# Optimization experiments

Hardware: AMD Instinct MI355X
Metric: run time of the kernel (lower is better)

The kernel has to match this reference:

```python
import jax, jax.numpy as jnp
import numpy as np

N_NODES = 50000
N_EDGES = 800000
D = 128


def setup_inputs() -> dict:
    key = jax.random.key(0)
    ks = jax.random.split(key, 8)
    x = jax.random.normal(ks[0], (N_NODES, D), dtype=jnp.float32)
    src = jax.random.randint(ks[1], (N_EDGES,), 0, N_NODES, dtype=jnp.int64)
    dst = jax.random.randint(ks[2], (N_EDGES,), 0, N_NODES, dtype=jnp.int64)
    edge_weights = jax.random.uniform(ks[3], (N_EDGES,), dtype=jnp.float32)
    scale = 1.0 / np.sqrt(D)
    W1 = jax.random.normal(ks[4], (D, D), dtype=jnp.float32) * scale
    b1 = jnp.zeros((D,), dtype=jnp.float32)
    W2 = jax.random.normal(ks[5], (D, D), dtype=jnp.float32) * scale
    b2 = jnp.zeros((D,), dtype=jnp.float32)
    return {"x": x, "src": src, "dst": dst, "edge_weights": edge_weights,
            "W1": W1, "b1": b1, "W2": W2, "b2": b2}


def reference(x, src, dst, edge_weights, W1, b1, W2, b2):
    n_nodes = x.shape[0]
    # out-degrees (edges where node is the source), clamped to >= 1
    deg = jax.ops.segment_sum(jnp.ones_like(src, dtype=x.dtype), src,
                              num_segments=n_nodes)
    deg = jnp.maximum(deg, 1.0)
    # per-edge symmetric-normalization coefficient: 1/sqrt(deg_u * deg_v)
    coef = jax.lax.rsqrt(deg[src] * deg[dst]) * edge_weights  # [E]
    # gather-multiply-scatter: sum_{u->v} x[u] * coef into node v
    msgs = x[src] * coef[:, None]                              # [E, D]
    agg = jax.ops.segment_sum(msgs, dst, num_segments=n_nodes)  # [N, D]
    # FFN: Linear -> ReLU -> Linear (dropout = 0)
    h = jax.nn.relu(agg @ W1 + b1)
    return h @ W2 + b2
```

## Files before the change

kernel.cpp:

```cpp
#include <hip/hip_runtime.h>

#define NN 50000
#define NE 800000
#define D  128
#define HB 128
#define CH 6272
#define PW 50176
#define XB 128
#define RB 49

typedef short short8 __attribute__((ext_vector_type(8)));
typedef float f32x4  __attribute__((ext_vector_type(4)));
typedef unsigned char u8;

__device__ __forceinline__ ushort f2bf(float f) {
    union { float f; unsigned u; } v; v.f = f;
    unsigned r = v.u + 0x7FFFu + ((v.u >> 16) & 1u);
    return (ushort)(r >> 16);
}


__global__ __launch_bounds__(1024) void prep_kernel(const int* __restrict__ src,
                                                    const int* __restrict__ dst,
                                                    const float* __restrict__ x,
                                                    const float* __restrict__ W1,
                                                    const float* __restrict__ W2,
                                                    u8* __restrict__ psrc,
                                                    u8* __restrict__ pdst,
                                                    ushort* __restrict__ xbf,
                                                    ushort* __restrict__ W1t,
                                                    ushort* __restrict__ W2t) {
    __shared__ unsigned bins[2 * PW / 4];
    const int t = threadIdx.x, b = blockIdx.x;

    if (b < HB) {
        for (int i = t; i < 2 * PW / 16; i += 1024)
            ((uint4*)bins)[i] = make_uint4(0, 0, 0, 0);
        __syncthreads();
        const int base = b * CH;
#pragma unroll
        for (int i = 0; i < 2; ++i) {
            int e0 = base + i * 4096 + t * 4;
            if (e0 < base + CH && e0 < NE) {
                int4 s4 = *(const int4*)(src + e0);
                int4 d4 = *(const int4*)(dst + e0);
                atomicAdd(&bins[s4.x >> 2], 1u << ((s4.x & 3) << 3));
                atomicAdd(&bins[s4.y >> 2], 1u << ((s4.y & 3) << 3));
                atomicAdd(&bins[s4.z >> 2], 1u << ((s4.z & 3) << 3));
                atomicAdd(&bins[s4.w >> 2], 1u << ((s4.w & 3) << 3));
                atomicAdd(&bins[PW / 4 + (d4.x >> 2)], 1u << ((d4.x & 3) << 3));
                atomicAdd(&bins[PW / 4 + (d4.y >> 2)], 1u << ((d4.y & 3) << 3));
                atomicAdd(&bins[PW / 4 + (d4.z >> 2)], 1u << ((d4.z & 3) << 3));
                atomicAdd(&bins[PW / 4 + (d4.w >> 2)], 1u << ((d4.w & 3) << 3));
            }
        }
        __syncthreads();
        uint4* os = (uint4*)(psrc + (size_t)b * PW);
        uint4* od = (uint4*)(pdst + (size_t)b * PW);
        for (int i = t; i < PW / 16; i += 1024) {
            os[i] = ((const uint4*)bins)[i];
            od[i] = ((const uint4*)(bins + PW / 4))[i];
        }
    } else if (b < HB + 4) {
        int c = (b - HB) * 1024 + t;
        if (c < 4096) {
            const float* W = (c < 2048) ? W1 : W2;
            ushort* Wt     = (c < 2048) ? W1t : W2t;
            int cc = c & 2047;
            int n  = cc >> 4;
            int k0 = (cc & 15) * 8;
            ushort tmp[8];
#pragma unroll
            for (int j = 0; j < 8; ++j) tmp[j] = f2bf(W[(k0 + j) * D + n]);
            *reinterpret_cast<uint4*>(Wt + n * D + k0) = *reinterpret_cast<uint4*>(tmp);
        }
    } else {
        for (int i = (b - HB - 4) * 1024 + t; i < NN * D / 8; i += XB * 1024) {
            const float4* p = (const float4*)(x + (size_t)i * 8);
            float4 v0 = p[0], v1 = p[1];
            ushort tmp[8];
            tmp[0] = f2bf(v0.x); tmp[1] = f2bf(v0.y); tmp[2] = f2bf(v0.z); tmp[3] = f2bf(v0.w);
            tmp[4] = f2bf(v1.x); tmp[5] = f2bf(v1.y); tmp[6] = f2bf(v1.z); tmp[7] = f2bf(v1.w);
            *reinterpret_cast<uint4*>(xbf + (size_t)i * 8) = *reinterpret_cast<uint4*>(tmp);
        }
    }
}

__global__ __launch_bounds__(256) void xprep_kernel(const float* __restrict__ x,
                                                    ushort* __restrict__ xbf) {
    int i = blockIdx.x * 256 + threadIdx.x;
    if (i >= NN * D / 8) return;
    const float4* p = (const float4*)(x + (size_t)i * 8);
    float4 v0 = p[0], v1 = p[1];
    ushort tmp[8];
    tmp[0] = f2bf(v0.x); tmp[1] = f2bf(v0.y); tmp[2] = f2bf(v0.z); tmp[3] = f2bf(v0.w);
    tmp[4] = f2bf(v1.x); tmp[5] = f2bf(v1.y); tmp[6] = f2bf(v1.z); tmp[7] = f2bf(v1.w);
    *reinterpret_cast<uint4*>(xbf + (size_t)i * 8) = *reinterpret_cast<uint4*>(tmp);
}


__global__ __launch_bounds__(256) void reduce_kernel(const unsigned* __restrict__ psrc32,
                                                     unsigned* __restrict__ pdst32,
                                                     float* __restrict__ rsq,
                                                     int* __restrict__ cnt,
                                                     int* __restrict__ bsum49) {
    __shared__ int sm[256];
    int t = threadIdx.x;
    int g = blockIdx.x * 256 + t;
    unsigned s02 = 0, s13 = 0;
    for (int b = 0; b < HB; ++b) {
        unsigned w = psrc32[(size_t)b * (PW / 4) + g];
        s02 += w & 0x00FF00FFu;
        s13 += (w >> 8) & 0x00FF00FFu;
    }
    unsigned r02 = 0, r13 = 0;
    for (int b = 0; b < HB; ++b) {
        size_t idx = (size_t)b * (PW / 4) + g;
        unsigned w = pdst32[idx];
        pdst32[idx] = (r02 & 0xFFu) | ((r13 & 0xFFu) << 8) |
                      (r02 & 0x00FF0000u) | ((r13 & 0x00FF0000u) << 8);
        r02 += w & 0x00FF00FFu;
        r13 += (w >> 8) & 0x00FF00FFu;
    }
    int v0 = g * 4;
    int dg[4] = { (int)(s02 & 0xFFFFu), (int)(s13 & 0xFFFFu),
                  (int)(s02 >> 16),     (int)(s13 >> 16) };
    int ct[4] = { (int)(r02 & 0xFFFFu), (int)(r13 & 0xFFFFu),
                  (int)(r02 >> 16),     (int)(r13 >> 16) };
    if (v0 + 3 < NN) {
        float4 rq = make_float4(rsqrtf(fmaxf((float)dg[0], 1.f)),
                                rsqrtf(fmaxf((float)dg[1], 1.f)),
                                rsqrtf(fmaxf((float)dg[2], 1.f)),
                                rsqrtf(fmaxf((float)dg[3], 1.f)));
        *(float4*)(rsq + v0) = rq;
        *(int4*)(cnt + v0) = make_int4(ct[0], ct[1], ct[2], ct[3]);
    } else {
        for (int j = 0; j < 4; ++j)
            if (v0 + j < NN) {
                rsq[v0 + j] = rsqrtf(fmaxf((float)dg[j], 1.f));
                cnt[v0 + j] = ct[j];
            }
    }
    int pad_ok = (v0 + 3 < NN);
    int mysum = pad_ok ? (ct[0] + ct[1] + ct[2] + ct[3]) : 0;
    if (!pad_ok)
        for (int j = 0; j < 4; ++j) if (v0 + j < NN) mysum += ct[j];
    sm[t] = mysum;
    __syncthreads();
    for (int s = 128; s > 0; s >>= 1) {
        if (t < s) sm[t] += sm[t + s];
        __syncthreads();
    }
    if (t == 0) bsum49[blockIdx.x] = sm[0];
}

__global__ __launch_bounds__(256) void scan_bsum(int* __restrict__ bsum49) {
    __shared__ int sm[256];
    int t = threadIdx.x;
    int v = (t < RB) ? bsum49[t] : 0;
    sm[t] = v;
    __syncthreads();
    for (int d2 = 1; d2 < 256; d2 <<= 1) {
        int u = (t >= d2) ? sm[t - d2] : 0;
        __syncthreads();
        sm[t] += u;
        __syncthreads();
    }
    if (t < RB) bsum49[t] = sm[t] - v;
}

__global__ __launch_bounds__(1024) void scan_write(const int* __restrict__ cnt,
                                                   const int* __restrict__ bsum49,
                                                   int* __restrict__ offs) {
    __shared__ int sm[1024];
    int b = blockIdx.x, t = threadIdx.x;
    int i = b * 1024 + t;
    int v = (i < NN) ? cnt[i] : 0;
    sm[t] = v;
    __syncthreads();
    for (int d2 = 1; d2 < 1024; d2 <<= 1) {
        int u = (t >= d2) ? sm[t - d2] : 0;
        __syncthreads();
        sm[t] += u;
        __syncthreads();
    }
    if (i < NN) offs[i] = bsum49[b] + sm[t] - v;
    if (b == 0 && t == 0) offs[NN] = NE;
}


__global__ __launch_bounds__(1024) void scatter_kernel(const int* __restrict__ src,
                                                       const int* __restrict__ dst,
                                                       const float* __restrict__ ew,
                                                       const float* __restrict__ rsq,
                                                       const int* __restrict__ offs,
                                                       const u8* __restrict__ pd,
                                                       unsigned* __restrict__ csr) {
    __shared__ unsigned cur[PW / 4];
    const int t = threadIdx.x, b = blockIdx.x;
    for (int i = t; i < PW / 16; i += 1024)
        ((uint4*)cur)[i] = make_uint4(0, 0, 0, 0);
    __syncthreads();

    const u8* pdrow = pd + (size_t)b * PW;
    const int base = b * CH;
#pragma unroll
    for (int i = 0; i < 2; ++i) {
        int e0 = base + i * 4096 + t * 4;
        if (e0 < base + CH && e0 < NE) {
            int4 s4 = *(const int4*)(src + e0);
            int4 d4 = *(const int4*)(dst + e0);
            float4 w4 = *(const float4*)(ew + e0);
#pragma unroll
            for (int j = 0; j < 4; ++j) {
                int s = (j == 0) ? s4.x : (j == 1) ? s4.y : (j == 2) ? s4.z : s4.w;
                int d = (j == 0) ? d4.x : (j == 1) ? d4.y : (j == 2) ? d4.z : d4.w;
                float w = (j == 0) ? w4.x : (j == 1) ? w4.y : (j == 2) ? w4.z : w4.w;
                int sh = (d & 3) << 3;
                unsigned old = atomicAdd(&cur[d >> 2], 1u << sh);
                int rel = (int)((old >> sh) & 0xFFu);
                int pos = offs[d] + (int)pdrow[d] + rel;
                float coef = rsq[s] * rsq[d] * w;
                csr[pos] = (unsigned)s | ((unsigned)f2bf(coef) << 16);
            }
        }
    }
}


__device__ __forceinline__ void acc_row(unsigned e, int lane,
                                        const ushort* __restrict__ xbf,
                                        float& a0, float& a1, float& a2, float& a3) {
    float c = __int_as_float(e & 0xFFFF0000u);
    uint2 u = ((const uint2*)(xbf + (size_t)(e & 0xFFFFu) * D))[lane];
    a0 = fmaf(__int_as_float((int)(u.x << 16)),        c, a0);
    a1 = fmaf(__int_as_float((int)(u.x & 0xFFFF0000u)), c, a1);
    a2 = fmaf(__int_as_float((int)(u.y << 16)),        c, a2);
    a3 = fmaf(__int_as_float((int)(u.y & 0xFFFF0000u)), c, a3);
}

__global__ __launch_bounds__(256) void gather_bf16_kernel(const int* __restrict__ offs,
                                                          const unsigned* __restrict__ csr,
                                                          const ushort* __restrict__ xbf,
                                                          float* __restrict__ agg) {
    int v = blockIdx.x * 8 + (threadIdx.x >> 5);
    if (v >= NN) return;
    int lane = threadIdx.x & 31;
    int beg = offs[v], end = offs[v + 1];
    float a0 = 0.f, a1 = 0.f, a2 = 0.f, a3 = 0.f;
    for (int i0 = beg; i0 < end; i0 += 32) {
        int n = end - i0; if (n > 32) n = 32;
        unsigned ej = (lane < n) ? csr[i0 + lane] : 0u;
        int j = 0;
        for (; j + 3 < n; j += 4) {
            unsigned e0 = __shfl(ej, j,     32);
            unsigned e1 = __shfl(ej, j + 1, 32);
            unsigned e2 = __shfl(ej, j + 2, 32);
            unsigned e3 = __shfl(ej, j + 3, 32);
            const uint2* r0 = (const uint2*)(xbf + (size_t)(e0 & 0xFFFFu) * D);
            const uint2* r1 = (const uint2*)(xbf + (size_t)(e1 & 0xFFFFu) * D);
            const uint2* r2 = (const uint2*)(xbf + (size_t)(e2 & 0xFFFFu) * D);
            const uint2* r3 = (const uint2*)(xbf + (size_t)(e3 & 0xFFFFu) * D);
            uint2 u0 = r0[lane], u1 = r1[lane], u2 = r2[lane], u3 = r3[lane];
            float c0 = __int_as_float(e0 & 0xFFFF0000u);
            float c1 = __int_as_float(e1 & 0xFFFF0000u);
            float c2 = __int_as_float(e2 & 0xFFFF0000u);
            float c3 = __int_as_float(e3 & 0xFFFF0000u);
            a0 = fmaf(__int_as_float((int)(u0.x << 16)),         c0, a0);
            a1 = fmaf(__int_as_float((int)(u0.x & 0xFFFF0000u)), c0, a1);
            a2 = fmaf(__int_as_float((int)(u0.y << 16)),         c0, a2);
            a3 = fmaf(__int_as_float((int)(u0.y & 0xFFFF0000u)), c0, a3);
            a0 = fmaf(__int_as_float((int)(u1.x << 16)),         c1, a0);
            a1 = fmaf(__int_as_float((int)(u1.x & 0xFFFF0000u)), c1, a1);
            a2 = fmaf(__int_as_float((int)(u1.y << 16)),         c1, a2);
            a3 = fmaf(__int_as_float((int)(u1.y & 0xFFFF0000u)), c1, a3);
            a0 = fmaf(__int_as_float((int)(u2.x << 16)),         c2, a0);
            a1 = fmaf(__int_as_float((int)(u2.x & 0xFFFF0000u)), c2, a1);
            a2 = fmaf(__int_as_float((int)(u2.y << 16)),         c2, a2);
            a3 = fmaf(__int_as_float((int)(u2.y & 0xFFFF0000u)), c2, a3);
            a0 = fmaf(__int_as_float((int)(u3.x << 16)),         c3, a0);
            a1 = fmaf(__int_as_float((int)(u3.x & 0xFFFF0000u)), c3, a1);
            a2 = fmaf(__int_as_float((int)(u3.y << 16)),         c3, a2);
            a3 = fmaf(__int_as_float((int)(u3.y & 0xFFFF0000u)), c3, a3);
        }
        for (; j < n; ++j) {
            unsigned e = __shfl(ej, j, 32);
            acc_row(e, lane, xbf, a0, a1, a2, a3);
        }
    }
    ((float4*)(agg + (size_t)v * D))[lane] = make_float4(a0, a1, a2, a3);
}


__global__ __launch_bounds__(256) void ffn_mfma_kernel(const float* __restrict__ agg,
                                                       const ushort* __restrict__ W1t,
                                                       const ushort* __restrict__ W2t,
                                                       const float* __restrict__ b1,
                                                       const float* __restrict__ b2,
                                                       float* __restrict__ out) {
    __shared__ ushort Wt[128 * 128];
    __shared__ ushort hS[4][16 * 128];

    const int t  = threadIdx.x;
    const int w  = t >> 6;
    const int l  = t & 63;
    const int lr = l & 15;
    const int lk = l >> 4;
    const int r0 = blockIdx.x * 64;

    for (int i = 0; i < 8; ++i) {
        int c = i * 256 + t;
        int n = c >> 4;
        int slot = c & 15;
        uint4 v = ((const uint4*)W1t)[c];
        int byte = n * 256 + ((slot * 16) ^ ((n & 7) << 4));
        *(uint4*)((char*)Wt + byte) = v;
    }

    const int arow = r0 + w * 16 + lr;
    short8 afrag[4];
#pragma unroll
    for (int kb = 0; kb < 4; ++kb) {
        int k = kb * 32 + lk * 8;
        float4 v0 = make_float4(0.f, 0.f, 0.f, 0.f), v1 = v0;
        if (arow < NN) {
            const float4* ap = (const float4*)(agg + (size_t)arow * D + k);
            v0 = ap[0]; v1 = ap[1];
        }
        short8 a;
        a[0] = (short)f2bf(v0.x); a[1] = (short)f2bf(v0.y);
        a[2] = (short)f2bf(v0.z); a[3] = (short)f2bf(v0.w);
        a[4] = (short)f2bf(v1.x); a[5] = (short)f2bf(v1.y);
        a[6] = (short)f2bf(v1.z); a[7] = (short)f2bf(v1.w);
        afrag[kb] = a;
    }
    __syncthreads();

    f32x4 acc[8];
#pragma unroll
    for (int nt = 0; nt < 8; ++nt) acc[nt] = (f32x4){0.f, 0.f, 0.f, 0.f};
#pragma unroll
    for (int kb = 0; kb < 4; ++kb) {
        int kbyte = (kb * 32 + lk * 8) * 2;
#pragma unroll
        for (int nt = 0; nt < 8; ++nt) {
            int n = nt * 16 + lr;
            short8 b = *(const short8*)((const char*)Wt + n * 256 + (kbyte ^ ((n & 7) << 4)));
            acc[nt] = __builtin_amdgcn_mfma_f32_16x16x32_bf16(afrag[kb], b, acc[nt], 0, 0, 0);
        }
    }
#pragma unroll
    for (int nt = 0; nt < 8; ++nt) {
        int col = nt * 16 + lr;
        float bb = b1[col];
#pragma unroll
        for (int r = 0; r < 4; ++r) {
            int row = lk * 4 + r;
            float h = fmaxf(acc[nt][r] + bb, 0.0f);
            int byte = row * 256 + ((col * 2) ^ ((row & 7) << 4));
            *(ushort*)((char*)&hS[w][0] + byte) = f2bf(h);
        }
    }
    __syncthreads();

    for (int i = 0; i < 8; ++i) {
        int c = i * 256 + t;
        int n = c >> 4;
        int slot = c & 15;
        uint4 v = ((const uint4*)W2t)[c];
        int byte = n * 256 + ((slot * 16) ^ ((n & 7) << 4));
        *(uint4*)((char*)Wt + byte) = v;
    }
    __syncthreads();

    short8 hfrag[4];
#pragma unroll
    for (int kb = 0; kb < 4; ++kb) {
        int kbyte = (kb * 32 + lk * 8) * 2;
        hfrag[kb] = *(const short8*)((const char*)&hS[w][0] + lr * 256 + (kbyte ^ ((lr & 7) << 4)));
    }
#pragma unroll
    for (int nt = 0; nt < 8; ++nt) acc[nt] = (f32x4){0.f, 0.f, 0.f, 0.f};
#pragma unroll
    for (int kb = 0; kb < 4; ++kb) {
        int kbyte = (kb * 32 + lk * 8) * 2;
#pragma unroll
        for (int nt = 0; nt < 8; ++nt) {
            int n = nt * 16 + lr;
            short8 b = *(const short8*)((const char*)Wt + n * 256 + (kbyte ^ ((n & 7) << 4)));
            acc[nt] = __builtin_amdgcn_mfma_f32_16x16x32_bf16(hfrag[kb], b, acc[nt], 0, 0, 0);
        }
    }
#pragma unroll
    for (int nt = 0; nt < 8; ++nt) {
        int col = nt * 16 + lr;
        float bb = b2[col];
#pragma unroll
        for (int r = 0; r < 4; ++r) {
            int row = r0 + w * 16 + lk * 4 + r;
            if (row < NN) out[(size_t)row * D + col] = acc[nt][r] + bb;
        }
    }
}


extern "C" void kernel_launch(void* const* d_in, const int* in_sizes, int n_in,
                              void* d_out, int out_size, void* d_ws, size_t ws_size,
                              hipStream_t stream) {
    const float* x  = (const float*)d_in[0];
    const int* src  = (const int*)d_in[1];
    const int* dst  = (const int*)d_in[2];
    const float* ew = (const float*)d_in[3];
    const float* W1 = (const float*)d_in[4];
    const float* b1 = (const float*)d_in[5];
    const float* W2 = (const float*)d_in[6];
    const float* b2 = (const float*)d_in[7];
    float* out = (float*)d_out;

    char* base = (char*)d_ws;
    size_t off = 0;
    auto alloc = [&](size_t bytes) { char* p = base + off; off = (off + bytes + 15) & ~(size_t)15; return p; };
    u8* psrc      = (u8*)alloc((size_t)HB * PW);
    u8* pdst      = (u8*)alloc((size_t)HB * PW);
    float* rsq    = (float*)alloc((size_t)NN * 4);
    int* cnt      = (int*)alloc((size_t)NN * 4);
    int* offs     = (int*)alloc((size_t)(NN + 1) * 4);
    int* bsum49   = (int*)alloc((size_t)RB * 4);
    unsigned* csr = (unsigned*)alloc((size_t)NE * 4);
    ushort* W1t   = (ushort*)alloc((size_t)D * D * 2);
    ushort* W2t   = (ushort*)alloc((size_t)D * D * 2);
    size_t off_noX = off;
    ushort* xbf_own = (ushort*)alloc((size_t)NN * D * 2);
    bool own_xbf = ws_size >= off;
    ushort* xbf = own_xbf ? xbf_own : (ushort*)psrc;
    (void)off_noX;

    int prep_grid = own_xbf ? (HB + 4 + XB) : (HB + 4);
    prep_kernel<<<prep_grid, 1024, 0, stream>>>(src, dst, x, W1, W2,
                                                psrc, pdst, xbf, W1t, W2t);
    reduce_kernel<<<RB, 256, 0, stream>>>((const unsigned*)psrc, (unsigned*)pdst,
                                          rsq, cnt, bsum49);
    scan_bsum<<<1, 256, 0, stream>>>(bsum49);
    scan_write<<<RB, 1024, 0, stream>>>(cnt, bsum49, offs);
    scatter_kernel<<<HB, 1024, 0, stream>>>(src, dst, ew, rsq, offs, pdst, csr);
    if (!own_xbf)
        xprep_kernel<<<(NN * D / 8 + 255) / 256, 256, 0, stream>>>(x, xbf);
    gather_bf16_kernel<<<(NN + 7) / 8, 256, 0, stream>>>(offs, csr, xbf, out);
    ffn_mfma_kernel<<<(NN + 63) / 64, 256, 0, stream>>>(out, W1t, W2t, b1, b2, out);
}
```

Measured before the change: 137.1 us.

## Parallelize histogram reduce, fuse block-sum scan, and partition gather by source range

The reduce kernel now splits each 4-node column across 8 threads, each handling 16 histogram rows, and combines them with sub-warp shuffle scans. This gives 8x more threads to hide the memory latency of the serial 128-row loops. The separate block-sum scan kernel is removed: each scan_write block sums the preceding block totals itself, saving one launch. The gather kernel now makes four passes over each node's edge list, each covering a quarter of the source-node range, to improve L2 locality of x rows. The cost is reading the CSR four times and serial ballot-driven loads that lose the previous 4-way load unrolling.

```diff
diff --git a/kernel.cpp b/kernel.cpp
--- a/kernel.cpp
+++ b/kernel.cpp
@@ -7,7 +7,8 @@
 #define CH 6272
 #define PW 50176
 #define XB 128
-#define RB 49
+#define RB2 98
+#define GRANGE 12544
 
 typedef short short8 __attribute__((ext_vector_type(8)));
 typedef float f32x4  __attribute__((ext_vector_type(4)));
@@ -99,92 +100,115 @@
 }
 
 
-__global__ __launch_bounds__(256) void reduce_kernel(const unsigned* __restrict__ psrc32,
-                                                     unsigned* __restrict__ pdst32,
-                                                     float* __restrict__ rsq,
-                                                     int* __restrict__ cnt,
-                                                     int* __restrict__ bsum49) {
-    __shared__ int sm[256];
-    int t = threadIdx.x;
-    int g = blockIdx.x * 256 + t;
-    unsigned s02 = 0, s13 = 0;
-    for (int b = 0; b < HB; ++b) {
-        unsigned w = psrc32[(size_t)b * (PW / 4) + g];
-        s02 += w & 0x00FF00FFu;
-        s13 += (w >> 8) & 0x00FF00FFu;
-    }
-    unsigned r02 = 0, r13 = 0;
-    for (int b = 0; b < HB; ++b) {
-        size_t idx = (size_t)b * (PW / 4) + g;
-        unsigned w = pdst32[idx];
-        pdst32[idx] = (r02 & 0xFFu) | ((r13 & 0xFFu) << 8) |
-                      (r02 & 0x00FF0000u) | ((r13 & 0x00FF0000u) << 8);
+__global__ __launch_bounds__(1024) void reduce_kernel(const unsigned* __restrict__ psrc32,
+                                                      unsigned* __restrict__ pdst32,
+                                                      float* __restrict__ rsq,
+                                                      int* __restrict__ cnt,
+                                                      int* __restrict__ bsum98) {
+    __shared__ int sm[128];
+    const int t = threadIdx.x;
+    const int g = (blockIdx.x * 1024 + t) >> 3;
+    const int c = t & 7;
+    const size_t stride = PW / 4;
+
+    unsigned wv[16];
+#pragma unroll
+    for (int i = 0; i < 16; ++i)
+        wv[i] = pdst32[(size_t)(c * 16 + i) * stride + g];
+    unsigned t02 = 0, t13 = 0;
+#pragma unroll
+    for (int i = 0; i < 16; ++i) {
+        t02 += wv[i] & 0x00FF00FFu;
+        t13 += (wv[i] >> 8) & 0x00FF00FFu;
+    }
+    unsigned p02 = 0, p13 = 0;
+#pragma unroll
+    for (int i = 0; i < 16; ++i) {
+        unsigned w = psrc32[(size_t)(c * 16 + i) * stride + g];
+        p02 += w & 0x00FF00FFu;
+        p13 += (w >> 8) & 0x00FF00FFu;
+    }
+    unsigned i02 = t02, i13 = t13;
+#pragma unroll
+    for (int off = 1; off < 8; off <<= 1) {
+        unsigned v02 = __shfl_up(i02, off, 8);
+        unsigned v13 = __shfl_up(i13, off, 8);
+        if (c >= off) { i02 += v02; i13 += v13; }
+    }
+    unsigned q02 = p02, q13 = p13, u02 = t02, u13 = t13;
+#pragma unroll
+    for (int off = 1; off < 8; off <<= 1) {
+        q02 += __shfl_xor(q02, off, 8);
+        q13 += __shfl_xor(q13, off, 8);
+        u02 += __shfl_xor(u02, off, 8);
+        u13 += __shfl_xor(u13, off, 8);
+    }
+    unsigned r02 = i02 - t02, r13 = i13 - t13;
+#pragma unroll
+    for (int i = 0; i < 16; ++i) {
+        unsigned w = wv[i];
+        pdst32[(size_t)(c * 16 + i) * stride + g] =
+            (r02 & 0xFFu) | ((r13 & 0xFFu) << 8) |
+            (r02 & 0x00FF0000u) | ((r13 & 0x00FF0000u) << 8);
         r02 += w & 0x00FF00FFu;
         r13 += (w >> 8) & 0x00FF00FFu;
     }
-    int v0 = g * 4;
-    int dg[4] = { (int)(s02 & 0xFFFFu), (int)(s13 & 0xFFFFu),
-                  (int)(s02 >> 16),     (int)(s13 >> 16) };
-    int ct[4] = { (int)(r02 & 0xFFFFu), (int)(r13 & 0xFFFFu),
-                  (int)(r02 >> 16),     (int)(r13 >> 16) };
-    if (v0 + 3 < NN) {
-        float4 rq = make_float4(rsqrtf(fmaxf((float)dg[0], 1.f)),
-                                rsqrtf(fmaxf((float)dg[1], 1.f)),
-                                rsqrtf(fmaxf((float)dg[2], 1.f)),
-                                rsqrtf(fmaxf((float)dg[3], 1.f)));
-        *(float4*)(rsq + v0) = rq;
-        *(int4*)(cnt + v0) = make_int4(ct[0], ct[1], ct[2], ct[3]);
-    } else {
-        for (int j = 0; j < 4; ++j)
-            if (v0 + j < NN) {
-                rsq[v0 + j] = rsqrtf(fmaxf((float)dg[j], 1.f));
-                cnt[v0 + j] = ct[j];
-            }
-    }
-    int pad_ok = (v0 + 3 < NN);
-    int mysum = pad_ok ? (ct[0] + ct[1] + ct[2] + ct[3]) : 0;
-    if (!pad_ok)
-        for (int j = 0; j < 4; ++j) if (v0 + j < NN) mysum += ct[j];
-    sm[t] = mysum;
-    __syncthreads();
-    for (int s = 128; s > 0; s >>= 1) {
+    int tct = 0;
+    if (c == 0) {
+        int v0 = g * 4;
+        int dg_[4] = { (int)(q02 & 0xFFFFu), (int)(q13 & 0xFFFFu),
+                       (int)(q02 >> 16),     (int)(q13 >> 16) };
+        int ct_[4] = { (int)(u02 & 0xFFFFu), (int)(u13 & 0xFFFFu),
+                       (int)(u02 >> 16),     (int)(u13 >> 16) };
+        tct = ct_[0] + ct_[1] + ct_[2] + ct_[3];
+        if (v0 + 3 < NN) {
+            *(float4*)(rsq + v0) = make_float4(rsqrtf(fmaxf((float)dg_[0], 1.f)),
+                                               rsqrtf(fmaxf((float)dg_[1], 1.f)),
+                                               rsqrtf(fmaxf((float)dg_[2], 1.f)),
+                                               rsqrtf(fmaxf((float)dg_[3], 1.f)));
+            *(int4*)(cnt + v0) = make_int4(ct_[0], ct_[1], ct_[2], ct_[3]);
+        } else {
+            for (int j = 0; j < 4; ++j)
+                if (v0 + j < NN) {
+                    rsq[v0 + j] = rsqrtf(fmaxf((float)dg_[j], 1.f));
+                    cnt[v0 + j] = ct_[j];
+                }
+        }
+        sm[t >> 3] = tct;
+    }
+    __syncthreads();
+    for (int s = 64; s > 0; s >>= 1) {
         if (t < s) sm[t] += sm[t + s];
         __syncthreads();
     }
-    if (t == 0) bsum49[blockIdx.x] = sm[0];
-}
-
-__global__ __launch_bounds__(256) void scan_bsum(int* __restrict__ bsum49) {
-    __shared__ int sm[256];
-    int t = threadIdx.x;
-    int v = (t < RB) ? bsum49[t] : 0;
-    sm[t] = v;
-    __syncthreads();
-    for (int d2 = 1; d2 < 256; d2 <<= 1) {
-        int u = (t >= d2) ? sm[t - d2] : 0;
-        __syncthreads();
-        sm[t] += u;
-        __syncthreads();
-    }
-    if (t < RB) bsum49[t] = sm[t] - v;
-}
-
-__global__ __launch_bounds__(1024) void scan_write(const int* __restrict__ cnt,
-                                                   const int* __restrict__ bsum49,
-                                                   int* __restrict__ offs) {
-    __shared__ int sm[1024];
-    int b = blockIdx.x, t = threadIdx.x;
-    int i = b * 1024 + t;
+    if (t == 0) bsum98[blockIdx.x] = sm[0];
+}
+
+
+__global__ __launch_bounds__(512) void scan_write(const int* __restrict__ cnt,
+                                                  const int* __restrict__ bsum98,
+                                                  int* __restrict__ offs) {
+    __shared__ int sm[512];
+    const int b = blockIdx.x, t = threadIdx.x;
+    sm[t] = (t < RB2 && t < b) ? bsum98[t] : 0;
+    __syncthreads();
+    for (int s = 256; s > 0; s >>= 1) {
+        if (t < s) sm[t] += sm[t + s];
+        __syncthreads();
+    }
+    int base = sm[0];
+    __syncthreads();
+    int i = b * 512 + t;
     int v = (i < NN) ? cnt[i] : 0;
     sm[t] = v;
     __syncthreads();
-    for (int d2 = 1; d2 < 1024; d2 <<= 1) {
+    for (int d2 = 1; d2 < 512; d2 <<= 1) {
         int u = (t >= d2) ? sm[t - d2] : 0;
         __syncthreads();
         sm[t] += u;
         __syncthreads();
     }
-    if (i < NN) offs[i] = bsum49[b] + sm[t] - v;
+    if (i < NN) offs[i] = base + sm[t] - v;
     if (b == 0 && t == 0) offs[NN] = NE;
 }
 
@@ -228,64 +252,34 @@
 }
 
 
-__device__ __forceinline__ void acc_row(unsigned e, int lane,
-                                        const ushort* __restrict__ xbf,
-                                        float& a0, float& a1, float& a2, float& a3) {
-    float c = __int_as_float(e & 0xFFFF0000u);
-    uint2 u = ((const uint2*)(xbf + (size_t)(e & 0xFFFFu) * D))[lane];
-    a0 = fmaf(__int_as_float((int)(u.x << 16)),        c, a0);
-    a1 = fmaf(__int_as_float((int)(u.x & 0xFFFF0000u)), c, a1);
-    a2 = fmaf(__int_as_float((int)(u.y << 16)),        c, a2);
-    a3 = fmaf(__int_as_float((int)(u.y & 0xFFFF0000u)), c, a3);
-}
-
 __global__ __launch_bounds__(256) void gather_bf16_kernel(const int* __restrict__ offs,
                                                           const unsigned* __restrict__ csr,
                                                           const ushort* __restrict__ xbf,
                                                           float* __restrict__ agg) {
     int v = blockIdx.x * 8 + (threadIdx.x >> 5);
     if (v >= NN) return;
-    int lane = threadIdx.x & 31;
-    int beg = offs[v], end = offs[v + 1];
+    const int lane = threadIdx.x & 31;
+    const int half = (threadIdx.x >> 5) & 1;
+    const int beg = offs[v], end = offs[v + 1];
     float a0 = 0.f, a1 = 0.f, a2 = 0.f, a3 = 0.f;
-    for (int i0 = beg; i0 < end; i0 += 32) {
-        int n = end - i0; if (n > 32) n = 32;
-        unsigned ej = (lane < n) ? csr[i0 + lane] : 0u;
-        int j = 0;
-        for (; j + 3 < n; j += 4) {
-            unsigned e0 = __shfl(ej, j,     32);
-            unsigned e1 = __shfl(ej, j + 1, 32);
-            unsigned e2 = __shfl(ej, j + 2, 32);
-            unsigned e3 = __shfl(ej, j + 3, 32);
-            const uint2* r0 = (const uint2*)(xbf + (size_t)(e0 & 0xFFFFu) * D);
-            const uint2* r1 = (const uint2*)(xbf + (size_t)(e1 & 0xFFFFu) * D);
-            const uint2* r2 = (const uint2*)(xbf + (size_t)(e2 & 0xFFFFu) * D);
-            const uint2* r3 = (const uint2*)(xbf + (size_t)(e3 & 0xFFFFu) * D);
-            uint2 u0 = r0[lane], u1 = r1[lane], u2 = r2[lane], u3 = r3[lane];
-            float c0 = __int_as_float(e0 & 0xFFFF0000u);
-            float c1 = __int_as_float(e1 & 0xFFFF0000u);
-            float c2 = __int_as_float(e2 & 0xFFFF0000u);
-            float c3 = __int_as_float(e3 & 0xFFFF0000u);
-            a0 = fmaf(__int_as_float((int)(u0.x << 16)),         c0, a0);
-            a1 = fmaf(__int_as_float((int)(u0.x & 0xFFFF0000u)), c0, a1);
-            a2 = fmaf(__int_as_float((int)(u0.y << 16)),         c0, a2);
-            a3 = fmaf(__int_as_float((int)(u0.y & 0xFFFF0000u)), c0, a3);
-            a0 = fmaf(__int_as_float((int)(u1.x << 16)),         c1, a0);
-            a1 = fmaf(__int_as_float((int)(u1.x & 0xFFFF0000u)), c1, a1);
-            a2 = fmaf(__int_as_float((int)(u1.y << 16)),         c1, a2);
-            a3 = fmaf(__int_as_float((int)(u1.y & 0xFFFF0000u)), c1, a3);
-            a0 = fmaf(__int_as_float((int)(u2.x << 16)),         c2, a0);
-            a1 = fmaf(__int_as_float((int)(u2.x & 0xFFFF0000u)), c2, a1);
-            a2 = fmaf(__int_as_float((int)(u2.y << 16)),         c2, a2);
-            a3 = fmaf(__int_as_float((int)(u2.y & 0xFFFF0000u)), c2, a3);
-            a0 = fmaf(__int_as_float((int)(u3.x << 16)),         c3, a0);
-            a1 = fmaf(__int_as_float((int)(u3.x & 0xFFFF0000u)), c3, a1);
-            a2 = fmaf(__int_as_float((int)(u3.y << 16)),         c3, a2);
-            a3 = fmaf(__int_as_float((int)(u3.y & 0xFFFF0000u)), c3, a3);
-        }
-        for (; j < n; ++j) {
-            unsigned e = __shfl(ej, j, 32);
-            acc_row(e, lane, xbf, a0, a1, a2, a3);
+#pragma unroll
+    for (int p = 0; p < 4; ++p) {
+        const unsigned lo = p * GRANGE;
+        for (int i0 = beg; i0 < end; i0 += 32) {
+            int n = end - i0; if (n > 32) n = 32;
+            unsigned ej = (lane < n) ? csr[i0 + lane] : 0u;
+            bool inr = (lane < n) && ((unsigned)(ej & 0xFFFFu) - lo < (unsigned)GRANGE);
+            unsigned m = (unsigned)(__ballot(inr) >> (half * 32));
+            while (m) {
+                int j = __builtin_ctz(m); m &= m - 1;
+                unsigned e = __shfl(ej, j, 32);
+                float c = __int_as_float(e & 0xFFFF0000u);
+                uint2 u = ((const uint2*)(xbf + (size_t)(e & 0xFFFFu) * D))[lane];
+                a0 = fmaf(__int_as_float((int)(u.x << 16)),         c, a0);
+                a1 = fmaf(__int_as_float((int)(u.x & 0xFFFF0000u)), c, a1);
+                a2 = fmaf(__int_as_float((int)(u.y << 16)),         c, a2);
+                a3 = fmaf(__int_as_float((int)(u.y & 0xFFFF0000u)), c, a3);
+            }
         }
     }
     ((float4*)(agg + (size_t)v * D))[lane] = make_float4(a0, a1, a2, a3);
@@ -425,23 +419,20 @@
     float* rsq    = (float*)alloc((size_t)NN * 4);
     int* cnt      = (int*)alloc((size_t)NN * 4);
     int* offs     = (int*)alloc((size_t)(NN + 1) * 4);
-    int* bsum49   = (int*)alloc((size_t)RB * 4);
+    int* bsum98   = (int*)alloc((size_t)RB2 * 4);
     unsigned* csr = (unsigned*)alloc((size_t)NE * 4);
     ushort* W1t   = (ushort*)alloc((size_t)D * D * 2);
     ushort* W2t   = (ushort*)alloc((size_t)D * D * 2);
-    size_t off_noX = off;
     ushort* xbf_own = (ushort*)alloc((size_t)NN * D * 2);
     bool own_xbf = ws_size >= off;
     ushort* xbf = own_xbf ? xbf_own : (ushort*)psrc;
-    (void)off_noX;
 
     int prep_grid = own_xbf ? (HB + 4 + XB) : (HB + 4);
     prep_kernel<<<prep_grid, 1024, 0, stream>>>(src, dst, x, W1, W2,
                                                 psrc, pdst, xbf, W1t, W2t);
-    reduce_kernel<<<RB, 256, 0, stream>>>((const unsigned*)psrc, (unsigned*)pdst,
-                                          rsq, cnt, bsum49);
-    scan_bsum<<<1, 256, 0, stream>>>(bsum49);
-    scan_write<<<RB, 1024, 0, stream>>>(cnt, bsum49, offs);
+    reduce_kernel<<<RB2, 1024, 0, stream>>>((const unsigned*)psrc, (unsigned*)pdst,
+                                            rsq, cnt, bsum98);
+    scan_write<<<RB2, 512, 0, stream>>>(cnt, bsum98, offs);
     scatter_kernel<<<HB, 1024, 0, stream>>>(src, dst, ew, rsq, offs, pdst, csr);
     if (!own_xbf)
         xprep_kernel<<<(NN * D / 8 + 255) / 256, 256, 0, stream>>>(x, xbf);
```

Result: slower. 141.7 us (+3.4%).
